# Performance work log

Measured on AMD Instinct MI355X. Metric: run time of the kernel, lower is better.

## Reference

```python
import jax, jax.numpy as jnp
import numpy as np

N_NODES = 50000


def _add_self_loops(edge_index, num_nodes):
    loop = jnp.arange(num_nodes, dtype=edge_index.dtype)
    row = jnp.concatenate([edge_index[0], loop])
    col = jnp.concatenate([edge_index[1], loop])
    return row, col


def _gcn_norm(row, col, num_nodes):
    # deg computed on target index with unit edge weights (PyG gcn_norm)
    deg = jax.ops.segment_sum(jnp.ones_like(col, dtype=jnp.float32), col,
                              num_segments=num_nodes)
    dis = jnp.where(deg > 0, jax.lax.rsqrt(jnp.maximum(deg, 1.0)), 0.0)
    return dis[row] * dis[col]  # [E]


def _gcn_conv(x, W, b, row, col, norm, num_nodes):
    h = x @ W                                  # dense transform first (PyG order)
    msg = h[row] * norm[:, None]               # gather + normalize
    out = jax.ops.segment_sum(msg, col, num_segments=num_nodes)  # scatter-add
    return out + b


def setup_inputs() -> dict:
    key = jax.random.key(0)
    ks = jax.random.split(key, 10)
    E = 800000
    x = jax.random.normal(ks[0], (N_NODES, 29), dtype=jnp.float32)
    edge_index = jax.random.randint(ks[1], (2, E), 0, N_NODES, dtype=jnp.int64)

    def glorot(k, fan_in, fan_out):
        s = jnp.sqrt(2.0 / (fan_in + fan_out)).astype(jnp.float32)
        return jax.random.normal(k, (fan_in, fan_out), dtype=jnp.float32) * s

    return {
        "x": x, "edge_index": edge_index,
        "W1": glorot(ks[2], 29, 96),  "b1": jnp.zeros((96,), jnp.float32),
        "W2": glorot(ks[3], 96, 128), "b2": jnp.zeros((128,), jnp.float32),
        "W3": glorot(ks[4], 128, 64), "b3": jnp.zeros((64,), jnp.float32),
        "W4": glorot(ks[5], 64, 32),  "b4": jnp.zeros((32,), jnp.float32),
    }


def reference(x, edge_index, W1, b1, W2, b2, W3, b3, W4, b4):
    row, col = _add_self_loops(edge_index, N_NODES)
    norm = _gcn_norm(row, col, N_NODES)  # same graph -> same norm for all layers
    h = _gcn_conv(x, W1, b1, row, col, norm, N_NODES)
    h = jax.nn.relu(h)
    # dropout(p=0.4) is identity in eval mode
    h = _gcn_conv(h, W2, b2, row, col, norm, N_NODES)
    h = _gcn_conv(h, W3, b3, row, col, norm, N_NODES)
    h = _gcn_conv(h, W4, b4, row, col, norm, N_NODES)
    return h
```

## Files before the change

### kernel.cpp

```cpp
#include <hip/hip_runtime.h>
#include <hip/hip_fp16.h>


constexpr int NN  = 50000;
constexpr int CAP = 64;
constexpr int CST = 32;
constexpr int AGB = (NN * 8 + 255) / 256;
constexpr int C1B = (NN + 255) / 256;
constexpr int PREPB = (NN * 32 + 64 + 255) / 256;
constexpr int W34XB = 17;
constexpr int W234XB = 13;
constexpr int PXB = 256;

typedef unsigned short u16;
typedef int iv4 __attribute__((ext_vector_type(4)));

__device__ __forceinline__ uint2 f4_to_h4(float4 v) {
    union { unsigned u; __half2 h; } a, b;
    a.h = __float22half2_rn(make_float2(v.x, v.y));
    b.h = __float22half2_rn(make_float2(v.z, v.w));
    return make_uint2(a.u, b.u);
}
__device__ __forceinline__ void h8_to_f8(uint4 g, float4& lo, float4& hi) {
    union { unsigned u; __half2 h; } t;
    float2 f;
    t.u = g.x; f = __half22float2(t.h); lo.x = f.x; lo.y = f.y;
    t.u = g.y; f = __half22float2(t.h); lo.z = f.x; lo.w = f.y;
    t.u = g.z; f = __half22float2(t.h); hi.x = f.x; hi.y = f.y;
    t.u = g.w; f = __half22float2(t.h); hi.z = f.x; hi.w = f.y;
}
__device__ __forceinline__ float4 f4add(float4 a, float4 b) {
    return make_float4(a.x + b.x, a.y + b.y, a.z + b.z, a.w + b.w);
}

__global__ void place_x_kernel(const int* __restrict__ row, const int* __restrict__ col,
                               int* __restrict__ cnt, u16* __restrict__ ell, int E) {
    const int g  = blockIdx.x & 7;
    const int bi = blockIdx.x >> 3;
    const int n4 = E >> 2;
    const int slice = (n4 + PXB - 1) / PXB;
    const int i0 = bi * slice;
    int i1 = i0 + slice; if (i1 > n4) i1 = n4;
    const iv4* cv = (const iv4*)col;
    const iv4* rv = (const iv4*)row;
#define PLACE1(cc, rr) {                                                        \
        const int c_ = (cc);                                                    \
        if ((((c_ >> 6) & 7) == g) && (unsigned)c_ < (unsigned)NN) {            \
            const int r_ = (rr);                                                \
            if ((unsigned)r_ < (unsigned)NN) {                                  \
                const int pos = atomicAdd(&cnt[(size_t)c_ * CST], 1);           \
                if (pos < CAP) ell[c_ * CAP + pos] = (u16)r_;                   \
            }                                                                   \
        }                                                                       \
    }
    for (int i = i0 + threadIdx.x; i < i1; i += 256) {
        const iv4 c4 = cv[i];
        const iv4 r4 = rv[i];
        PLACE1(c4.x, r4.x);
        PLACE1(c4.y, r4.y);
        PLACE1(c4.z, r4.z);
        PLACE1(c4.w, r4.w);
    }
    if (bi == 0) {
        for (int e = (n4 << 2) + threadIdx.x; e < E; e += 256) {
            const int c = col[e];
            if (((c >> 6) & 7) != g || (unsigned)c >= (unsigned)NN) continue;
            const int r = row[e];
            if ((unsigned)r >= (unsigned)NN) continue;
            const int pos = atomicAdd(&cnt[(size_t)c * CST], 1);
            if (pos < CAP) ell[c * CAP + pos] = (u16)r;
        }
    }
#undef PLACE1
}

__global__ void prep_all_kernel(const int* __restrict__ cnt, u16* __restrict__ ell,
                                const float* __restrict__ x, float* __restrict__ dis,
                                u16* __restrict__ mq,
                                unsigned* __restrict__ Xh,
                                unsigned* __restrict__ Ha, unsigned* __restrict__ Hb,
                                float* __restrict__ c1d,
                                const float* __restrict__ W3, const float* __restrict__ W4,
                                const float* __restrict__ b3,
                                float* __restrict__ W34, float* __restrict__ v1) {
    if (blockIdx.x >= PREPB) {
        const int wid = (blockIdx.x - PREPB) * 256 + threadIdx.x;
        if (wid < 4096) {
            const int r = wid >> 5, j = wid & 31;
            float a = 0.f;
#pragma unroll 8
            for (int k = 0; k < 64; ++k) a = fmaf(W3[r * 64 + k], W4[k * 32 + j], a);
            W34[wid] = a;
        } else if (wid < 4128) {
            const int j = wid - 4096;
            float a = 0.f;
#pragma unroll 8
            for (int k = 0; k < 64; ++k) a = fmaf(b3[k], W4[k * 32 + j], a);
            v1[j] = a;
        }
        return;
    }
    const int idx = blockIdx.x * blockDim.x + threadIdx.x;
    if (idx < NN * 32) {
        const int n = idx >> 5, f = idx & 31;
        int m = cnt[(size_t)n * CST]; if (m > CAP) m = CAP;
        const float d = rsqrtf((float)m + 1.0f);
        const float val = (f < 29) ? x[n * 29 + f] * d : 0.f;
        ((__half*)Xh)[idx] = __float2half(val);
        if (f == 31) dis[n] = d;
        if (f == 30) {
            int mp = (m + 7) & ~7; if (mp > CAP) mp = CAP;
            for (int k = m; k < mp; ++k) ell[n * CAP + k] = (u16)NN;
        }
        if (f == 29) mq[n] = (u16)((m + 7) >> 3);
    } else {
        const int i = idx - NN * 32;
        if (i < 16) {
            Xh[NN * 16 + i] = 0u; Ha[NN * 16 + i] = 0u; Hb[NN * 16 + i] = 0u;
        }
        if (i == 32) dis[NN] = 0.f;
        else if (i == 33) c1d[NN] = 0.f;
    }
}

template<int MODE>
__device__ __forceinline__ void agg32h_body(const uint4* __restrict__ hh,
                                            const u16* __restrict__ mq,
                                            const u16* __restrict__ ell,
                                            const float* __restrict__ dis,
                                            const float* __restrict__ c1,
                                            const float* __restrict__ c2,
                                            const float* __restrict__ v1,
                                            const float* __restrict__ v2,
                                            const float* __restrict__ bv,
                                            void* __restrict__ out) {
    const int idx = blockIdx.x * blockDim.x + threadIdx.x;
    if (idx >= NN * 8) return;
    const int n = idx >> 3, c = idx & 7;
    const int q = c & 3;
    const int h = c >> 2;
    const uint4* hp = hh + q;
    float4 aL, aH;
    {
        float4 sl, sh;
        h8_to_f8(hp[(size_t)n * 4], sl, sh);
        const float m0 = h ? 0.f : 1.f;
        aL = make_float4(sl.x * m0, sl.y * m0, sl.z * m0, sl.w * m0);
        aH = make_float4(sh.x * m0, sh.y * m0, sh.z * m0, sh.w * m0);
    }
    const int m8 = mq[n];
    const int4* ip = (const int4*)(ell + (size_t)n * CAP);
    int t = 0;
    for (; t + 2 <= m8; t += 2) {
        const int4 sA = ip[t], sB = ip[t + 1];
        const unsigned a0 = (unsigned)sA.x, a1 = (unsigned)sA.y;
        const unsigned a2 = (unsigned)sA.z, a3 = (unsigned)sA.w;
        const unsigned b0 = (unsigned)sB.x, b1 = (unsigned)sB.y;
        const unsigned b2 = (unsigned)sB.z, b3 = (unsigned)sB.w;
        const unsigned i0 = h ? (a0 >> 16) : (a0 & 0xFFFFu);
        const unsigned i1 = h ? (a1 >> 16) : (a1 & 0xFFFFu);
        const unsigned i2 = h ? (a2 >> 16) : (a2 & 0xFFFFu);
        const unsigned i3 = h ? (a3 >> 16) : (a3 & 0xFFFFu);
        const unsigned i4 = h ? (b0 >> 16) : (b0 & 0xFFFFu);
        const unsigned i5 = h ? (b1 >> 16) : (b1 & 0xFFFFu);
        const unsigned i6 = h ? (b2 >> 16) : (b2 & 0xFFFFu);
        const unsigned i7 = h ? (b3 >> 16) : (b3 & 0xFFFFu);
        const uint4 g0 = hp[(size_t)i0 * 4], g1 = hp[(size_t)i1 * 4];
        const uint4 g2 = hp[(size_t)i2 * 4], g3 = hp[(size_t)i3 * 4];
        const uint4 g4 = hp[(size_t)i4 * 4], g5 = hp[(size_t)i5 * 4];
        const uint4 g6 = hp[(size_t)i6 * 4], g7 = hp[(size_t)i7 * 4];
        float4 l0, h0, l1, h1, l2, h2, l3, h3, l4, h4, l5, h5, l6, h6, l7, h7;
        h8_to_f8(g0, l0, h0); h8_to_f8(g1, l1, h1);
        h8_to_f8(g2, l2, h2); h8_to_f8(g3, l3, h3);
        h8_to_f8(g4, l4, h4); h8_to_f8(g5, l5, h5);
        h8_to_f8(g6, l6, h6); h8_to_f8(g7, l7, h7);
        aL = f4add(aL, f4add(f4add(f4add(l0, l1), f4add(l2, l3)),
                             f4add(f4add(l4, l5), f4add(l6, l7))));
        aH = f4add(aH, f4add(f4add(f4add(h0, h1), f4add(h2, h3)),
                             f4add(f4add(h4, h5), f4add(h6, h7))));
    }
    if (t < m8) {
        const int4 s = ip[t];
        const unsigned w0 = (unsigned)s.x, w1 = (unsigned)s.y;
        const unsigned w2 = (unsigned)s.z, w3 = (unsigned)s.w;
        const unsigned i0 = h ? (w0 >> 16) : (w0 & 0xFFFFu);
        const unsigned i1 = h ? (w1 >> 16) : (w1 & 0xFFFFu);
        const unsigned i2 = h ? (w2 >> 16) : (w2 & 0xFFFFu);
        const unsigned i3 = h ? (w3 >> 16) : (w3 & 0xFFFFu);
        const uint4 g0 = hp[(size_t)i0 * 4], g1 = hp[(size_t)i1 * 4];
        const uint4 g2 = hp[(size_t)i2 * 4], g3 = hp[(size_t)i3 * 4];
        float4 l0, h0, l1, h1, l2, h2, l3, h3;
        h8_to_f8(g0, l0, h0); h8_to_f8(g1, l1, h1);
        h8_to_f8(g2, l2, h2); h8_to_f8(g3, l3, h3);
        aL = f4add(aL, f4add(f4add(l0, l1), f4add(l2, l3)));
        aH = f4add(aH, f4add(f4add(h0, h1), f4add(h2, h3)));
    }
    aL.x += __shfl_xor(aL.x, 4); aL.y += __shfl_xor(aL.y, 4);
    aL.z += __shfl_xor(aL.z, 4); aL.w += __shfl_xor(aL.w, 4);
    aH.x += __shfl_xor(aH.x, 4); aH.y += __shfl_xor(aH.y, 4);
    aH.z += __shfl_xor(aH.z, 4); aH.w += __shfl_xor(aH.w, 4);
    const float d = dis[n];
    if (MODE == 1) {
        if (c < 4) {
            const float d2 = d * d;
            float4 rl = make_float4(aL.x * d2, aL.y * d2, aL.z * d2, aL.w * d2);
            float4 rh = make_float4(aH.x * d2, aH.y * d2, aH.z * d2, aH.w * d2);
            const uint2 pl = f4_to_h4(rl), ph = f4_to_h4(rh);
            uint4 o; o.x = pl.x; o.y = pl.y; o.z = ph.x; o.w = ph.y;
            ((uint4*)out)[(size_t)n * 4 + q] = o;
        }
    } else {
        const int lane = threadIdx.x & 63;
        const int src = (lane & ~7) | (c >> 1);
        const float s0 = __shfl(aL.x, src), s1 = __shfl(aL.y, src);
        const float s2 = __shfl(aL.z, src), s3 = __shfl(aL.w, src);
        const float s4 = __shfl(aH.x, src), s5 = __shfl(aH.y, src);
        const float s6 = __shfl(aH.z, src), s7 = __shfl(aH.w, src);
        const float4 acc = (c & 1) ? make_float4(s4, s5, s6, s7)
                                   : make_float4(s0, s1, s2, s3);
        float4 r;
        if (MODE == 0) {
            r.x = acc.x * d; r.y = acc.y * d; r.z = acc.z * d; r.w = acc.w * d;
        } else {
            const float a1 = c1[n], a2 = c2[n];
            const float4 w1 = ((const float4*)v1)[c];
            const float4 w2 = ((const float4*)v2)[c];
            const float4 bb = ((const float4*)bv)[c];
            r.x = fmaf(acc.x, d, fmaf(a1, w1.x, fmaf(a2, w2.x, bb.x)));
            r.y = fmaf(acc.y, d, fmaf(a1, w1.y, fmaf(a2, w2.y, bb.y)));
            r.z = fmaf(acc.z, d, fmaf(a1, w1.z, fmaf(a2, w2.z, bb.z)));
            r.w = fmaf(acc.w, d, fmaf(a1, w1.w, fmaf(a2, w2.w, bb.w)));
        }
        ((float4*)out)[idx] = r;
    }
}

__device__ __forceinline__ void agg1_body(const float* __restrict__ in,
                                          const u16* __restrict__ mq,
                                          const u16* __restrict__ ell,
                                          const float* __restrict__ dis,
                                          float* __restrict__ out,
                                          float* __restrict__ outd, int blk0) {
    const int n = (blockIdx.x - blk0) * 256 + threadIdx.x;
    if (n >= NN) return;
    float acc = in[n];
    const int m8 = mq[n];
    const iv4* ip = (const iv4*)(ell + (size_t)n * CAP);
    for (int t = 0; t < m8; ++t) {
        const iv4 s = ip[t];
        const unsigned ux = (unsigned)s.x, uy = (unsigned)s.y;
        const unsigned uz = (unsigned)s.z, uw = (unsigned)s.w;
        acc += ((in[ux & 0xFFFFu] + in[ux >> 16]) + (in[uy & 0xFFFFu] + in[uy >> 16]))
             + ((in[uz & 0xFFFFu] + in[uz >> 16]) + (in[uw & 0xFFFFu] + in[uw >> 16]));
    }
    const float r = dis[n] * acc;
    out[n] = r;
    if (outd) outd[n] = r * dis[n];
}

__global__ void agg_pre_kernel(const uint4* __restrict__ Xh, const u16* __restrict__ mq,
                               const u16* __restrict__ ell, const float* __restrict__ dis,
                               float* __restrict__ Bb, float* __restrict__ c1,
                               float* __restrict__ c1d,
                               const float* __restrict__ W2, const float* __restrict__ b2,
                               const float* __restrict__ W34, float* __restrict__ W234,
                               float* __restrict__ v2) {
    if (blockIdx.x < AGB) {
        agg32h_body<0>(Xh, mq, ell, dis, nullptr, nullptr, nullptr, nullptr, nullptr, Bb);
    } else if (blockIdx.x < AGB + C1B) {
        agg1_body(dis, mq, ell, dis, c1, c1d, AGB);
    } else {
        const int wid = (blockIdx.x - AGB - C1B) * 256 + threadIdx.x;
        if (wid < 3072) {
            const int r = wid >> 5, j = wid & 31;
            float a = 0.f;
#pragma unroll 8
            for (int k = 0; k < 128; ++k) a = fmaf(W2[r * 128 + k], W34[k * 32 + j], a);
            W234[wid] = a;
        } else if (wid < 3104) {
            const int j = wid - 3072;
            float a = 0.f;
#pragma unroll 8
            for (int k = 0; k < 128; ++k) a = fmaf(b2[k], W34[k * 32 + j], a);
            v2[j] = a;
        }
    }
}

__global__ void agg_hop1_kernel(const uint4* __restrict__ Ha, const u16* __restrict__ mq,
                                const u16* __restrict__ ell, const float* __restrict__ dis,
                                uint4* __restrict__ Hb, const float* __restrict__ c1d,
                                float* __restrict__ c2) {
    if (blockIdx.x < AGB)
        agg32h_body<1>(Ha, mq, ell, dis, nullptr, nullptr, nullptr, nullptr, nullptr, Hb);
    else
        agg1_body(c1d, mq, ell, dis, c2, nullptr, AGB);
}

__global__ void agg_hop2_kernel(const uint4* __restrict__ Hb, const u16* __restrict__ mq,
                                const u16* __restrict__ ell, const float* __restrict__ dis,
                                uint4* __restrict__ Ha) {
    agg32h_body<1>(Hb, mq, ell, dis, nullptr, nullptr, nullptr, nullptr, nullptr, Ha);
}

__global__ void agg_hop3_kernel(const uint4* __restrict__ Ha, const u16* __restrict__ mq,
                                const u16* __restrict__ ell, const float* __restrict__ dis,
                                const float* __restrict__ c1, const float* __restrict__ c2,
                                const float* __restrict__ v1, const float* __restrict__ v2,
                                const float* __restrict__ bv, float* __restrict__ out) {
    agg32h_body<2>(Ha, mq, ell, dis, c1, c2, v1, v2, bv, out);
}

__global__ void __launch_bounds__(192, 2)
gemm_fused_kernel(const float* __restrict__ X, const float* __restrict__ W1,
                  const float* __restrict__ b1, const float* __restrict__ dis,
                  const float* __restrict__ W234, uint2* __restrict__ G) {
    constexpr int NPB = 16, RSX = 36, RSH = 104;
    __shared__ float xs[NPB * RSX];
    __shared__ float hsm[NPB * RSH];
    const int tid = threadIdx.x;
    const int n0  = blockIdx.x * NPB;

    const float4* Xv = (const float4*)(X + (size_t)n0 * 32);
    for (int i = tid; i < NPB * 8; i += 192) {
        const int nl = i >> 3, r = i & 7;
        float4 v = make_float4(0.f, 0.f, 0.f, 0.f);
        if (n0 + nl < NN) v = Xv[nl * 8 + r];
        *(float4*)(xs + nl * RSX + r * 4) = v;
    }
    __syncthreads();

    {
        const int cg = tid % 24, g = tid / 24;
        const float* x0 = xs + (2 * g) * RSX;
        const float* x1 = x0 + RSX;
        const float4* Wv = (const float4*)W1;
        float4 a0 = make_float4(0.f, 0.f, 0.f, 0.f);
        float4 a1 = make_float4(0.f, 0.f, 0.f, 0.f);
#pragma unroll
        for (int k = 0; k < 29; ++k) {
            const float4 w = Wv[k * 24 + cg];
            const float v0 = x0[k], v1 = x1[k];
            a0.x = fmaf(v0, w.x, a0.x); a0.y = fmaf(v0, w.y, a0.y);
            a0.z = fmaf(v0, w.z, a0.z); a0.w = fmaf(v0, w.w, a0.w);
            a1.x = fmaf(v1, w.x, a1.x); a1.y = fmaf(v1, w.y, a1.y);
            a1.z = fmaf(v1, w.z, a1.z); a1.w = fmaf(v1, w.w, a1.w);
        }
        const float4 bb = ((const float4*)b1)[cg];
#pragma unroll
        for (int h = 0; h < 2; ++h) {
            const int nl = 2 * g + h, node = n0 + nl;
            const float d = (node < NN) ? dis[node] : 0.f;
            const float4 a = h ? a1 : a0;
            float4 r;
            r.x = fmaxf(a.x + bb.x, 0.f) * d; r.y = fmaxf(a.y + bb.y, 0.f) * d;
            r.z = fmaxf(a.z + bb.z, 0.f) * d; r.w = fmaxf(a.w + bb.w, 0.f) * d;
            *(float4*)(hsm + nl * RSH + cg * 4) = r;
        }
    }
    __syncthreads();

    if (tid < 128) {
        const int nl = tid >> 3, cg = tid & 7;
        const float* hr = hsm + nl * RSH;
        const float4* Wv = (const float4*)W234;
        float4 a = make_float4(0.f, 0.f, 0.f, 0.f);
#pragma unroll 8
        for (int k = 0; k < 96; ++k) {
            const float4 w = Wv[k * 8 + cg];
            const float v = hr[k];
            a.x = fmaf(v, w.x, a.x); a.y = fmaf(v, w.y, a.y);
            a.z = fmaf(v, w.z, a.z); a.w = fmaf(v, w.w, a.w);
        }
        const int node = n0 + nl;
        if (node < NN) G[(size_t)node * 8 + cg] = f4_to_h4(a);
    }
}

extern "C" void kernel_launch(void* const* d_in, const int* in_sizes, int n_in,
                              void* d_out, int out_size, void* d_ws, size_t ws_size,
                              hipStream_t stream) {
    const float* x  = (const float*)d_in[0];
    const int*   ei = (const int*)d_in[1];
    const float* W1 = (const float*)d_in[2]; const float* b1 = (const float*)d_in[3];
    const float* W2 = (const float*)d_in[4]; const float* b2 = (const float*)d_in[5];
    const float* W3 = (const float*)d_in[6]; const float* b3 = (const float*)d_in[7];
    const float* W4 = (const float*)d_in[8]; const float* b4p = (const float*)d_in[9];
    float* outp = (float*)d_out;

    const int E = in_sizes[1] / 2;
    const int* row = ei;
    const int* col = ei + E;

    int*   cnt  = (int*)d_ws;
    float* dis  = (float*)(cnt + 50048 * CST);
    u16*   ell  = (u16*)(dis + 50064);
    u16*   mq   = (u16*)((int*)ell + 1600000);
    float* c1   = (float*)((int*)mq + 25024);
    float* c1d  = c1 + 50064;
    float* c2   = c1d + 50064;
    float* W34  = c2 + 50064;
    float* W234 = W34 + 4096;
    float* v1   = W234 + 3072;
    float* v2   = v1 + 32;
    unsigned* Xh = (unsigned*)(v2 + 32);
    float* Bb   = (float*)(Xh + 800032);
    unsigned* Ha = (unsigned*)(Bb + 1600064);
    unsigned* Hb = Ha + 800032;

    hipMemsetAsync(cnt, 0, (size_t)50048 * CST * sizeof(int), stream);
    place_x_kernel<<<8 * PXB, 256, 0, stream>>>(row, col, cnt, ell, E);
    prep_all_kernel<<<PREPB + W34XB, 256, 0, stream>>>(cnt, ell, x, dis, mq, Xh,
                                                       Ha, Hb, c1d, W3, W4, b3, W34, v1);
    agg_pre_kernel<<<AGB + C1B + W234XB, 256, 0, stream>>>((const uint4*)Xh, mq, ell, dis,
                                                           Bb, c1, c1d,
                                                           W2, b2, W34, W234, v2);
    gemm_fused_kernel<<<(NN + 15) / 16, 192, 0, stream>>>(Bb, W1, b1, dis, W234,
                                                          (uint2*)Ha);
    agg_hop1_kernel<<<AGB + C1B, 256, 0, stream>>>((const uint4*)Ha, mq, ell, dis,
                                                   (uint4*)Hb, c1d, c2);
    agg_hop2_kernel<<<AGB, 256, 0, stream>>>((const uint4*)Hb, mq, ell, dis, (uint4*)Ha);
    agg_hop3_kernel<<<AGB, 256, 0, stream>>>((const uint4*)Ha, mq, ell, dis,
                                             c1, c2, v1, v2, b4p, outp);
}
```

Before: 207.2 us.

## Aggregate edge placement counts in LDS before global atomics

The edge placement kernel now splits nodes into 16 groups and 8 edge slices per group, 128 blocks of 512 threads. Each block first counts its edges per target node in shared memory, then reserves a range of slots in each node's global counter with one atomicAdd, then reads the edges a second time and writes them to ELL positions taken from a shared-memory cursor. This replaces one global atomic per edge with one per (block, node) pair. The cost is reading the edge arrays twice, and with only 128 blocks the GPU may be under-occupied.

```diff
diff --git a/kernel.cpp b/kernel.cpp
--- a/kernel.cpp
+++ b/kernel.cpp
@@ -10,7 +10,9 @@
 constexpr int PREPB = (NN * 32 + 64 + 255) / 256;
 constexpr int W34XB = 17;
 constexpr int W234XB = 13;
-constexpr int PXB = 256;
+constexpr int PGRP = 16;
+constexpr int PNB  = 8;
+constexpr int LRANGE = 3136;
 
 typedef unsigned short u16;
 typedef int iv4 __attribute__((ext_vector_type(4)));
@@ -33,45 +35,80 @@
     return make_float4(a.x + b.x, a.y + b.y, a.z + b.z, a.w + b.w);
 }
 
-__global__ void place_x_kernel(const int* __restrict__ row, const int* __restrict__ col,
-                               int* __restrict__ cnt, u16* __restrict__ ell, int E) {
-    const int g  = blockIdx.x & 7;
-    const int bi = blockIdx.x >> 3;
+__global__ void __launch_bounds__(512)
+place_lds_kernel(const int* __restrict__ row, const int* __restrict__ col,
+                 int* __restrict__ cnt, u16* __restrict__ ell, int E) {
+    __shared__ unsigned lcnt[LRANGE];
+    __shared__ unsigned lpos[LRANGE];
+    const int gg = blockIdx.x & 15;
+    const int b  = blockIdx.x >> 4;
     const int n4 = E >> 2;
-    const int slice = (n4 + PXB - 1) / PXB;
-    const int i0 = bi * slice;
+    const int slice = (n4 + PNB - 1) / PNB;
+    const int i0 = b * slice;
     int i1 = i0 + slice; if (i1 > n4) i1 = n4;
     const iv4* cv = (const iv4*)col;
     const iv4* rv = (const iv4*)row;
-#define PLACE1(cc, rr) {                                                        \
+
+    for (int i = threadIdx.x; i < LRANGE; i += 512) { lcnt[i] = 0u; lpos[i] = 0u; }
+    __syncthreads();
+
+#define KEEPC(cc, rr, body) {                                                   \
         const int c_ = (cc);                                                    \
-        if ((((c_ >> 6) & 7) == g) && (unsigned)c_ < (unsigned)NN) {            \
+        if ((((c_ >> 6) & 15) == gg) && (unsigned)c_ < (unsigned)NN) {          \
             const int r_ = (rr);                                                \
-            if ((unsigned)r_ < (unsigned)NN) {                                  \
-                const int pos = atomicAdd(&cnt[(size_t)c_ * CST], 1);           \
-                if (pos < CAP) ell[c_ * CAP + pos] = (u16)r_;                   \
-            }                                                                   \
+            if ((unsigned)r_ < (unsigned)NN) { body }                           \
         }                                                                       \
     }
-    for (int i = i0 + threadIdx.x; i < i1; i += 256) {
+    for (int i = i0 + threadIdx.x; i < i1; i += 512) {
         const iv4 c4 = cv[i];
         const iv4 r4 = rv[i];
-        PLACE1(c4.x, r4.x);
-        PLACE1(c4.y, r4.y);
-        PLACE1(c4.z, r4.z);
-        PLACE1(c4.w, r4.w);
-    }
-    if (bi == 0) {
-        for (int e = (n4 << 2) + threadIdx.x; e < E; e += 256) {
+        KEEPC(c4.x, r4.x, { const int lc = ((c_ >> 10) << 6) | (c_ & 63);
+                            atomicAdd(&lcnt[lc], 1u); })
+        KEEPC(c4.y, r4.y, { const int lc = ((c_ >> 10) << 6) | (c_ & 63);
+                            atomicAdd(&lcnt[lc], 1u); })
+        KEEPC(c4.z, r4.z, { const int lc = ((c_ >> 10) << 6) | (c_ & 63);
+                            atomicAdd(&lcnt[lc], 1u); })
+        KEEPC(c4.w, r4.w, { const int lc = ((c_ >> 10) << 6) | (c_ & 63);
+                            atomicAdd(&lcnt[lc], 1u); })
+    }
+    if (b == 0) {
+        for (int e = (n4 << 2) + threadIdx.x; e < E; e += 512) {
             const int c = col[e];
-            if (((c >> 6) & 7) != g || (unsigned)c >= (unsigned)NN) continue;
+            if (((c >> 6) & 15) != gg || (unsigned)c >= (unsigned)NN) continue;
             const int r = row[e];
             if ((unsigned)r >= (unsigned)NN) continue;
             const int pos = atomicAdd(&cnt[(size_t)c * CST], 1);
             if (pos < CAP) ell[c * CAP + pos] = (u16)r;
         }
     }
-#undef PLACE1
+    __syncthreads();
+
+    for (int lc = threadIdx.x; lc < LRANGE; lc += 512) {
+        const unsigned cv_ = lcnt[lc];
+        if (cv_) {
+            const int c = ((lc >> 6) << 10) | (gg << 6) | (lc & 63);
+            lcnt[lc] = (unsigned)atomicAdd(&cnt[(size_t)c * CST], (int)cv_);
+        }
+    }
+    __syncthreads();
+
+    for (int i = i0 + threadIdx.x; i < i1; i += 512) {
+        const iv4 c4 = cv[i];
+        const iv4 r4 = rv[i];
+        KEEPC(c4.x, r4.x, { const int lc = ((c_ >> 10) << 6) | (c_ & 63);
+                            const unsigned gp = lcnt[lc] + atomicAdd(&lpos[lc], 1u);
+                            if (gp < CAP) ell[c_ * CAP + gp] = (u16)r_; })
+        KEEPC(c4.y, r4.y, { const int lc = ((c_ >> 10) << 6) | (c_ & 63);
+                            const unsigned gp = lcnt[lc] + atomicAdd(&lpos[lc], 1u);
+                            if (gp < CAP) ell[c_ * CAP + gp] = (u16)r_; })
+        KEEPC(c4.z, r4.z, { const int lc = ((c_ >> 10) << 6) | (c_ & 63);
+                            const unsigned gp = lcnt[lc] + atomicAdd(&lpos[lc], 1u);
+                            if (gp < CAP) ell[c_ * CAP + gp] = (u16)r_; })
+        KEEPC(c4.w, r4.w, { const int lc = ((c_ >> 10) << 6) | (c_ & 63);
+                            const unsigned gp = lcnt[lc] + atomicAdd(&lpos[lc], 1u);
+                            if (gp < CAP) ell[c_ * CAP + gp] = (u16)r_; })
+    }
+#undef KEEPC
 }
 
 __global__ void prep_all_kernel(const int* __restrict__ cnt, u16* __restrict__ ell,
@@ -409,7 +446,7 @@
     unsigned* Hb = Ha + 800032;
 
     hipMemsetAsync(cnt, 0, (size_t)50048 * CST * sizeof(int), stream);
-    place_x_kernel<<<8 * PXB, 256, 0, stream>>>(row, col, cnt, ell, E);
+    place_lds_kernel<<<PGRP * PNB, 512, 0, stream>>>(row, col, cnt, ell, E);
     prep_all_kernel<<<PREPB + W34XB, 256, 0, stream>>>(cnt, ell, x, dis, mq, Xh,
                                                        Ha, Hb, c1d, W3, W4, b3, W34, v1);
     agg_pre_kernel<<<AGB + C1B + W234XB, 256, 0, stream>>>((const uint4*)Xh, mq, ell, dis,
```

Result: slower. 248.1 us (+19.7%).
